# Kernel optimization log

Hardware: AMD Instinct MI355X
Metric: run time of the kernel (lower is better)

## Reference

```python
import jax, jax.numpy as jnp
import numpy as np

B, C, T, V, H = 128, 128, 64, 25, 4
EPS = 1e-5


def _bn(x, g, b, m, v):
    # eval-mode BatchNorm2d over channel axis 1 of [B,C,T,V]
    inv = g / jnp.sqrt(v + EPS)
    return x * inv[:, None, None] + (b - m * inv)[:, None, None]


def setup_inputs() -> dict:
    key = jax.random.key(0)
    ks = jax.random.split(key, 12)
    s = 0.05
    return {
        "x": jax.random.normal(ks[0], (B, C, T, V), jnp.float32),
        "bn0_gamma": jnp.ones((C,), jnp.float32),
        "bn0_beta": jnp.zeros((C,), jnp.float32),
        "bn0_mean": jax.random.normal(ks[1], (C,), jnp.float32) * s,
        "bn0_var": jnp.abs(jax.random.normal(ks[2], (C,), jnp.float32)) + 1.0,
        "conv1_w": jax.random.normal(ks[3], (2 * C, C), jnp.float32) * (1.0 / np.sqrt(C)),
        "conv1_b": jax.random.normal(ks[4], (2 * C,), jnp.float32) * s,
        "bn1_gamma": jnp.ones((C,), jnp.float32),
        "bn1_beta": jnp.zeros((C,), jnp.float32),
        "bn1_mean": jax.random.normal(ks[5], (C,), jnp.float32) * s,
        "bn1_var": jnp.abs(jax.random.normal(ks[6], (C,), jnp.float32)) + 1.0,
        "bn2_gamma": jnp.ones((C,), jnp.float32),
        "bn2_beta": jnp.zeros((C,), jnp.float32),
        "bn2_mean": jax.random.normal(ks[7], (C,), jnp.float32) * s,
        "bn2_var": jnp.abs(jax.random.normal(ks[8], (C,), jnp.float32)) + 1.0,
        "shared_topology": jnp.tile(jnp.eye(V, dtype=jnp.float32)[None], (H, 1, 1))
                           + jax.random.normal(ks[9], (H, V, V), jnp.float32) * s,
        "spatial_weight": jax.random.normal(ks[10], (H, V, V), jnp.float32) * s,
        "conv2_w": jax.random.normal(ks[11], (C, C), jnp.float32) * (1.0 / np.sqrt(C)),
        "conv2_b": jnp.zeros((C,), jnp.float32),
    }


def reference(x, bn0_gamma, bn0_beta, bn0_mean, bn0_var,
              conv1_w, conv1_b,
              bn1_gamma, bn1_beta, bn1_mean, bn1_var,
              bn2_gamma, bn2_beta, bn2_mean, bn2_var,
              shared_topology, spatial_weight,
              conv2_w, conv2_b):
    residual = x
    h = _bn(x, bn0_gamma, bn0_beta, bn0_mean, bn0_var)
    # conv1: 1x1 conv C -> 2C
    h = jnp.einsum('oc,bctv->botv', conv1_w, h) + conv1_b[None, :, None, None]
    h = jax.nn.gelu(h, approximate=False)  # torch nn.GELU default is exact
    z1, z2 = jnp.split(h, 2, axis=1)
    z1 = _bn(z1, bn1_gamma, bn1_beta, bn1_mean, bn1_var)
    z2 = _bn(z2, bn2_gamma, bn2_beta, bn2_mean, bn2_var)
    D = C // H
    z1 = z1.reshape(B, H, D, T, V)
    z2 = z2.reshape(B, H, D, T, V)
    y1 = jnp.einsum('huv,bhdtv->bhdtu', shared_topology, z1)
    attn = jnp.einsum('huv,bhdtv->bhdtu', spatial_weight, z2)
    y = (y1 + z1 * attn).reshape(B, C, T, V)
    y = jnp.einsum('oc,bctv->botv', conv2_w, y) + conv2_b[None, :, None, None]
    return jax.nn.relu(y + residual)
```

## Files before the change

### kernel.cpp

```cpp
#include <hip/hip_runtime.h>
#include <math.h>

#define C_   128
#define T_   64
#define V_   25
#define TV   1600
#define CTV  204800
#define EPS  1e-5f
#define TT   2
#define HS   136
#define ZS   72
#define RSZ  9216

typedef __bf16 bf16x8 __attribute__((ext_vector_type(8)));
typedef __bf16 bf16x4 __attribute__((ext_vector_type(4)));
typedef float  f32x4  __attribute__((ext_vector_type(4)));

__device__ __forceinline__ float gelu_exact(float x) {
  float y = fabsf(x) * 0.70710678118654752440f;
  float t = __builtin_amdgcn_rcpf(fmaf(0.47047f, y, 1.0f));
  float p = fmaf(0.7478556f, t, -0.0958798f);
  p = fmaf(p, t, 0.3480242f);
  p = p * t;
  float s = p * __expf(-y * y);
  float hxs = 0.5f * x * s;
  return x >= 0.0f ? x - hxs : hxs;
}

__global__ __launch_bounds__(256) void prep_pack(
    const float* __restrict__ W1, const float* __restrict__ W2,
    const float* __restrict__ topo, const float* __restrict__ spat,
    const float* __restrict__ b1,
    const float* __restrict__ bn0g, const float* __restrict__ bn0b,
    const float* __restrict__ bn0m, const float* __restrict__ bn0v,
    const float* __restrict__ bn1g, const float* __restrict__ bn1b,
    const float* __restrict__ bn1m, const float* __restrict__ bn1v,
    const float* __restrict__ bn2g, const float* __restrict__ bn2b,
    const float* __restrict__ bn2m, const float* __restrict__ bn2v,
    __bf16* __restrict__ W1p, __bf16* __restrict__ W2p, __bf16* __restrict__ Sp,
    float* __restrict__ b1a, float* __restrict__ binv, float* __restrict__ badd) {
  if (blockIdx.x == 128) {
    int o = threadIdx.x;
    float acc = b1[o];
    for (int c = 0; c < 128; ++c) {
      float inv = bn0g[c] * rsqrtf(bn0v[c] + EPS);
      float add = fmaf(-bn0m[c], inv, bn0b[c]);
      acc = fmaf(W1[o * 128 + c], add, acc);
    }
    b1a[o] = acc;
    float g, bb, m, vv;
    if (o < 128) { g = bn1g[o]; bb = bn1b[o]; m = bn1m[o]; vv = bn1v[o]; }
    else { int c = o - 128; g = bn2g[c]; bb = bn2b[c]; m = bn2m[c]; vv = bn2v[c]; }
    float inv = g * rsqrtf(vv + EPS);
    binv[o] = inv;
    badd[o] = fmaf(-m, inv, bb);
    return;
  }
  int i = blockIdx.x * 256 + threadIdx.x;
  if (i < 32768) {
    int j = i & 7, l = (i >> 3) & 63, ks = (i >> 9) & 3, ot = i >> 11;
    int o = ot * 16 + (l & 15);
    int c = ks * 32 + ((l >> 4) << 3) + j;
    float inv = bn0g[c] * rsqrtf(bn0v[c] + EPS);
    W1p[i] = (__bf16)(W1[o * 128 + c] * inv);
  }
  if (i < 16384) {
    int j = i & 7, l = (i >> 3) & 63, ks = (i >> 9) & 3, ot = i >> 11;
    int o = ot * 16 + (l & 15);
    int c = ks * 32 + ((l >> 4) << 3) + j;
    W2p[i] = (__bf16)W2[o * 128 + c];
  }
  if (i < 8192) {
    int j = i & 7, l = (i >> 3) & 63, ut = (i >> 9) & 1, mat = (i >> 10) & 1, h = i >> 11;
    int u = ut * 16 + (l & 15);
    int v = ((l >> 4) << 3) + j;
    const float* src = mat ? spat : topo;
    Sp[i] = (__bf16)((u < 25 && v < 25) ? src[h * 625 + u * 25 + v] : 0.0f);
  }
}


__device__ __forceinline__ void p0_stage(__bf16* hT, const float* xb, int tid) {
  const int c = tid >> 2, q = tid & 3;
  const int t = q & 1, vh = q >> 1;
  const float* xr = xb + c * TV + t * V_;
  const int v0 = vh * 12;
  float xv[13];
  #pragma unroll
  for (int i = 0; i < 13; ++i) xv[i] = xr[v0 + i];
  #pragma unroll
  for (int i = 0; i < 13; ++i)
    hT[(t * 32 + v0 + i) * HS + c] = (__bf16)xv[i];
}

__device__ __forceinline__ void conv1_mfma(const __bf16* hT, const __bf16* W1p,
    int wave, int lane, int lr, int lg, float bv0, float bv1, f32x4 acc[2][4]) {
  #pragma unroll
  for (int mt = 0; mt < 4; ++mt) {
    acc[0][mt] = f32x4{bv0, bv0, bv0, bv0};
    acc[1][mt] = f32x4{bv1, bv1, bv1, bv1};
  }
  #pragma unroll
  for (int ks = 0; ks < 4; ++ks) {
    bf16x8 ah[4];
    #pragma unroll
    for (int mt = 0; mt < 4; ++mt)
      ah[mt] = *reinterpret_cast<const bf16x8*>(&hT[(mt * 16 + lr) * HS + ks * 32 + lg * 8]);
    #pragma unroll
    for (int nt = 0; nt < 2; ++nt) {
      bf16x8 bw = *reinterpret_cast<const bf16x8*>(W1p + (((wave * 2 + nt) * 4 + ks) << 9) + lane * 8);
      #pragma unroll
      for (int mt = 0; mt < 4; ++mt)
        acc[nt][mt] = __builtin_amdgcn_mfma_f32_16x16x32_bf16(ah[mt], bw, acc[nt][mt], 0, 0, 0);
    }
  }
}

__device__ __forceinline__ void gelu_epi(const f32x4 acc[2][4], __bf16* z1, __bf16* z2,
    int wave, int lg, int o0, float inv0, float add0, float inv1, float add1) {
  __bf16* zdst = (wave < 4) ? z1 : z2;
  #pragma unroll
  for (int nt = 0; nt < 2; ++nt) {
    const float inv = nt ? inv1 : inv0;
    const float add = nt ? add1 : add0;
    const int orow = (o0 + nt * 16) & 127;
    #pragma unroll
    for (int mt = 0; mt < 4; ++mt) {
      bf16x4 pk;
      #pragma unroll
      for (int r = 0; r < 4; ++r) {
        int v = ((mt & 1) * 16) + lg * 4 + r;
        float z = fmaf(gelu_exact(acc[nt][mt][r]), inv, add);
        pk[r] = (v < V_) ? (__bf16)z : (__bf16)0.0f;
      }
      *reinterpret_cast<bf16x4*>(zdst + orow * ZS + mt * 16 + lg * 4) = pk;
    }
  }
}

__device__ __forceinline__ void spatial_mfma(const __bf16* z1, const __bf16* z2,
    const bf16x8 at0, const bf16x8 at1, const bf16x8 as0, const bf16x8 as1,
    int cbase, int lr, int lg, float yv[2][2][4]) {
  f32x4 accY[2][2] = {}, accA[2][2] = {};
  #pragma unroll
  for (int t = 0; t < 2; ++t) {
    bf16x8 az1 = *reinterpret_cast<const bf16x8*>(&z1[(cbase + lr) * ZS + t * 32 + lg * 8]);
    bf16x8 az2 = *reinterpret_cast<const bf16x8*>(&z2[(cbase + lr) * ZS + t * 32 + lg * 8]);
    accY[0][t] = __builtin_amdgcn_mfma_f32_16x16x32_bf16(az1, at0, accY[0][t], 0, 0, 0);
    accY[1][t] = __builtin_amdgcn_mfma_f32_16x16x32_bf16(az1, at1, accY[1][t], 0, 0, 0);
    accA[0][t] = __builtin_amdgcn_mfma_f32_16x16x32_bf16(az2, as0, accA[0][t], 0, 0, 0);
    accA[1][t] = __builtin_amdgcn_mfma_f32_16x16x32_bf16(az2, as1, accA[1][t], 0, 0, 0);
  }
  #pragma unroll
  for (int ut = 0; ut < 2; ++ut) {
    const int u = ut * 16 + lr;
    #pragma unroll
    for (int t = 0; t < 2; ++t)
      #pragma unroll
      for (int r = 0; r < 4; ++r) {
        const int c = cbase + lg * 4 + r;
        float z1u = (float)z1[c * ZS + t * 32 + u];
        yv[ut][t][r] = fmaf(z1u, accA[ut][t][r], accY[ut][t][r]);
      }
  }
}

__device__ __forceinline__ void p2_store(const float yv[2][2][4], __bf16* yT,
    int cbase, int lr, int lg) {
  #pragma unroll
  for (int ut = 0; ut < 2; ++ut)
    #pragma unroll
    for (int t = 0; t < 2; ++t) {
      const int row = t * 32 + ut * 16 + lr;
      bf16x4 pk;
      #pragma unroll
      for (int r = 0; r < 4; ++r) pk[r] = (__bf16)yv[ut][t][r];
      *reinterpret_cast<bf16x4*>(yT + row * HS + cbase + lg * 4) = pk;
    }
}

__device__ __forceinline__ void conv2_mfma(const __bf16* yT, const __bf16* W2p,
    int wave, int lane, int lr, int lg, const f32x4 bv2q, f32x4 acc2[4]) {
  #pragma unroll
  for (int n4 = 0; n4 < 4; ++n4) acc2[n4] = bv2q;
  #pragma unroll
  for (int ks = 0; ks < 4; ++ks) {
    bf16x8 af = *reinterpret_cast<const bf16x8*>(W2p + ((wave * 4 + ks) << 9) + lane * 8);
    #pragma unroll
    for (int n4 = 0; n4 < 4; ++n4) {
      bf16x8 ay = *reinterpret_cast<const bf16x8*>(&yT[(n4 * 16 + lr) * HS + ks * 32 + lg * 8]);
      acc2[n4] = __builtin_amdgcn_mfma_f32_16x16x32_bf16(af, ay, acc2[n4], 0, 0, 0);
    }
  }
}

__device__ __forceinline__ void p3_store(const f32x4 acc2[4], const float* xb,
    float* ob, int wave, int lr, int lg) {
  #pragma unroll
  for (int n4 = 0; n4 < 4; ++n4) {
    const int col = n4 * 16 + lr;
    const int t = col >> 5, u = col & 31;
    if (u < V_) {
      #pragma unroll
      for (int r = 0; r < 4; ++r) {
        const int o = wave * 16 + lg * 4 + r;
        const int off = o * TV + t * V_ + u;
        ob[off] = fmaxf(acc2[n4][r] + xb[off], 0.0f);
      }
    }
  }
}

__global__ __launch_bounds__(512, 4) void fused_v16(
    const float* __restrict__ x, const float* __restrict__ b2,
    const __bf16* __restrict__ W1p, const __bf16* __restrict__ W2p,
    const __bf16* __restrict__ Sp,
    const float* __restrict__ b1a, const float* __restrict__ binv,
    const float* __restrict__ badd,
    float* __restrict__ out) {
  __shared__ __bf16 sR[4 * RSZ];
  __bf16* RA = sR;
  __bf16* RB = sR + RSZ;
  __bf16* RC = sR + 2 * RSZ;
  __bf16* RD = sR + 3 * RSZ;

  const int hw = blockIdx.x;
  const int pb = (hw & 7) * 256 + (hw >> 3);
  const int b  = pb >> 4;
  const int tb0 = (pb & 15) * 2;
  const float* xb0 = x   + (size_t)b * CTV + tb0 * (TT * V_);
  float*       ob0 = out + (size_t)b * CTV + tb0 * (TT * V_);
  const float* xb1 = xb0 + TT * V_;
  float*       ob1 = ob0 + TT * V_;
  const int tid  = threadIdx.x;
  const int wave = tid >> 6, lane = tid & 63;
  const int lr = lane & 15, lg = lane >> 4;

  const int o0 = wave * 32 + lr;
  const float bv1a0 = b1a[o0], bv1a1 = b1a[o0 + 16];
  const float inv0 = binv[o0], add0 = badd[o0];
  const float inv1 = binv[o0 + 16], add1 = badd[o0 + 16];
  const f32x4 bv2q = *reinterpret_cast<const f32x4*>(b2 + wave * 16 + lg * 4);
  const int h2 = wave >> 1, ch = wave & 1;
  const int cbase = h2 * 32 + ch * 16;
  const bf16x8 at0 = *reinterpret_cast<const bf16x8*>(Sp + (((h2 * 2 + 0) * 2 + 0) << 9) + lane * 8);
  const bf16x8 at1 = *reinterpret_cast<const bf16x8*>(Sp + (((h2 * 2 + 0) * 2 + 1) << 9) + lane * 8);
  const bf16x8 as0 = *reinterpret_cast<const bf16x8*>(Sp + (((h2 * 2 + 1) * 2 + 0) << 9) + lane * 8);
  const bf16x8 as1 = *reinterpret_cast<const bf16x8*>(Sp + (((h2 * 2 + 1) * 2 + 1) << 9) + lane * 8);

  f32x4 acc[2][4];
  f32x4 acc2[4];
  float yv[2][2][4];

  p0_stage(RA, xb0, tid);
  __syncthreads();

  conv1_mfma(RA, W1p, wave, lane, lr, lg, bv1a0, bv1a1, acc);
  gelu_epi(acc, RC, RD, wave, lg, o0, inv0, add0, inv1, add1);
  __syncthreads();

  spatial_mfma(RC, RD, at0, at1, as0, as1, cbase, lr, lg, yv);
  p0_stage(RA, xb1, tid);
  p2_store(yv, RB, cbase, lr, lg);
  __syncthreads();

  conv2_mfma(RB, W2p, wave, lane, lr, lg, bv2q, acc2);
  conv1_mfma(RA, W1p, wave, lane, lr, lg, bv1a0, bv1a1, acc);
  gelu_epi(acc, RC, RD, wave, lg, o0, inv0, add0, inv1, add1);
  p3_store(acc2, xb0, ob0, wave, lr, lg);
  __syncthreads();

  spatial_mfma(RC, RD, at0, at1, as0, as1, cbase, lr, lg, yv);
  p2_store(yv, RB, cbase, lr, lg);
  __syncthreads();

  conv2_mfma(RB, W2p, wave, lane, lr, lg, bv2q, acc2);
  p3_store(acc2, xb1, ob1, wave, lr, lg);
}

extern "C" void kernel_launch(void* const* d_in, const int* in_sizes, int n_in,
                              void* d_out, int out_size, void* d_ws, size_t ws_size,
                              hipStream_t stream) {
  const float* x    = (const float*)d_in[0];
  const float* bn0g = (const float*)d_in[1];
  const float* bn0b = (const float*)d_in[2];
  const float* bn0m = (const float*)d_in[3];
  const float* bn0v = (const float*)d_in[4];
  const float* W1   = (const float*)d_in[5];
  const float* b1   = (const float*)d_in[6];
  const float* bn1g = (const float*)d_in[7];
  const float* bn1b = (const float*)d_in[8];
  const float* bn1m = (const float*)d_in[9];
  const float* bn1v = (const float*)d_in[10];
  const float* bn2g = (const float*)d_in[11];
  const float* bn2b = (const float*)d_in[12];
  const float* bn2m = (const float*)d_in[13];
  const float* bn2v = (const float*)d_in[14];
  const float* topo = (const float*)d_in[15];
  const float* spat = (const float*)d_in[16];
  const float* W2   = (const float*)d_in[17];
  const float* b2   = (const float*)d_in[18];
  float* out = (float*)d_out;

  __bf16* W1p = (__bf16*)d_ws;
  __bf16* W2p = W1p + 32768;
  __bf16* Sp  = W2p + 16384;
  float*  b1a  = (float*)((char*)d_ws + 114688);
  float*  binv = b1a + 256;
  float*  badd = binv + 256;

  prep_pack<<<129, 256, 0, stream>>>(W1, W2, topo, spat, b1,
                                     bn0g, bn0b, bn0m, bn0v,
                                     bn1g, bn1b, bn1m, bn1v,
                                     bn2g, bn2b, bn2m, bn2v,
                                     W1p, W2p, Sp, b1a, binv, badd);
  fused_v16<<<2048, 512, 0, stream>>>(
      x, b2, W1p, W2p, Sp, b1a, binv, badd, out);
}
```

Measured before the change: 99.41 us.

## Make blocks persistent over four tile pairs with a pipelined loop

Each block now loops over four consecutive pairs of time tiles instead of one pair, with grid reduced from 2048 to 512 blocks. The next tile's input staging is overlapped with the previous tile's conv2/store phase across loop iterations. This amortizes per-block setup (bias, BN and spatial-weight register loads, pipeline fill) but cuts resident blocks per CU and thus latency hiding. Address swizzling of blocks is dropped in favor of contiguous quarter-batch chunks.

Result: slower. 275.2 us (+176.8%).

```diff
diff --git a/kernel.cpp b/kernel.cpp
--- a/kernel.cpp
+++ b/kernel.cpp
@@ -211,7 +211,7 @@
   }
 }
 
-__global__ __launch_bounds__(512, 4) void fused_v16(
+__global__ __launch_bounds__(512, 4) void fused_v17(
     const float* __restrict__ x, const float* __restrict__ b2,
     const __bf16* __restrict__ W1p, const __bf16* __restrict__ W2p,
     const __bf16* __restrict__ Sp,
@@ -224,14 +224,11 @@
   __bf16* RC = sR + 2 * RSZ;
   __bf16* RD = sR + 3 * RSZ;
 
-  const int hw = blockIdx.x;
-  const int pb = (hw & 7) * 256 + (hw >> 3);
-  const int b  = pb >> 4;
-  const int tb0 = (pb & 15) * 2;
-  const float* xb0 = x   + (size_t)b * CTV + tb0 * (TT * V_);
-  float*       ob0 = out + (size_t)b * CTV + tb0 * (TT * V_);
-  const float* xb1 = xb0 + TT * V_;
-  float*       ob1 = ob0 + TT * V_;
+  const int qb   = blockIdx.x;
+  const int b    = qb >> 2;
+  const int quad = qb & 3;
+  const float* xq = x   + (size_t)b * CTV + quad * (16 * V_);
+  float*       oq = out + (size_t)b * CTV + quad * (16 * V_);
   const int tid  = threadIdx.x;
   const int wave = tid >> 6, lane = tid & 63;
   const int lr = lane & 15, lg = lane >> 4;
@@ -248,34 +245,56 @@
   const bf16x8 as0 = *reinterpret_cast<const bf16x8*>(Sp + (((h2 * 2 + 1) * 2 + 0) << 9) + lane * 8);
   const bf16x8 as1 = *reinterpret_cast<const bf16x8*>(Sp + (((h2 * 2 + 1) * 2 + 1) << 9) + lane * 8);
 
-  f32x4 acc[2][4];
-  f32x4 acc2[4];
-  float yv[2][2][4];
-
-  p0_stage(RA, xb0, tid);
+  p0_stage(RA, xq, tid);
   __syncthreads();
 
-  conv1_mfma(RA, W1p, wave, lane, lr, lg, bv1a0, bv1a1, acc);
-  gelu_epi(acc, RC, RD, wave, lg, o0, inv0, add0, inv1, add1);
-  __syncthreads();
-
-  spatial_mfma(RC, RD, at0, at1, as0, as1, cbase, lr, lg, yv);
-  p0_stage(RA, xb1, tid);
-  p2_store(yv, RB, cbase, lr, lg);
-  __syncthreads();
-
-  conv2_mfma(RB, W2p, wave, lane, lr, lg, bv2q, acc2);
-  conv1_mfma(RA, W1p, wave, lane, lr, lg, bv1a0, bv1a1, acc);
-  gelu_epi(acc, RC, RD, wave, lg, o0, inv0, add0, inv1, add1);
-  p3_store(acc2, xb0, ob0, wave, lr, lg);
-  __syncthreads();
-
-  spatial_mfma(RC, RD, at0, at1, as0, as1, cbase, lr, lg, yv);
-  p2_store(yv, RB, cbase, lr, lg);
-  __syncthreads();
-
-  conv2_mfma(RB, W2p, wave, lane, lr, lg, bv2q, acc2);
-  p3_store(acc2, xb1, ob1, wave, lr, lg);
+  #pragma unroll 1
+  for (int i = 0; i < 4; ++i) {
+    const float* xt0 = xq + i * (2 * TT * V_);
+    float*       ot0 = oq + i * (2 * TT * V_);
+    const float* xt1 = xt0 + TT * V_;
+    float*       ot1 = ot0 + TT * V_;
+
+    {
+      f32x4 acc[2][4];
+      conv1_mfma(RA, W1p, wave, lane, lr, lg, bv1a0, bv1a1, acc);
+      gelu_epi(acc, RC, RD, wave, lg, o0, inv0, add0, inv1, add1);
+    }
+    __syncthreads();
+
+    {
+      float yv[2][2][4];
+      spatial_mfma(RC, RD, at0, at1, as0, as1, cbase, lr, lg, yv);
+      p0_stage(RA, xt1, tid);
+      p2_store(yv, RB, cbase, lr, lg);
+    }
+    __syncthreads();
+
+    {
+      f32x4 acc2[4];
+      f32x4 acc[2][4];
+      conv2_mfma(RB, W2p, wave, lane, lr, lg, bv2q, acc2);
+      conv1_mfma(RA, W1p, wave, lane, lr, lg, bv1a0, bv1a1, acc);
+      gelu_epi(acc, RC, RD, wave, lg, o0, inv0, add0, inv1, add1);
+      p3_store(acc2, xt0, ot0, wave, lr, lg);
+    }
+    __syncthreads();
+
+    {
+      float yv[2][2][4];
+      spatial_mfma(RC, RD, at0, at1, as0, as1, cbase, lr, lg, yv);
+      p2_store(yv, RB, cbase, lr, lg);
+    }
+    __syncthreads();
+
+    {
+      f32x4 acc2[4];
+      conv2_mfma(RB, W2p, wave, lane, lr, lg, bv2q, acc2);
+      if (i < 3) p0_stage(RA, xt1 + TT * V_, tid);
+      p3_store(acc2, xt1, ot1, wave, lr, lg);
+    }
+    if (i < 3) __syncthreads();
+  }
 }
 
 extern "C" void kernel_launch(void* const* d_in, const int* in_sizes, int n_in,
@@ -314,6 +333,6 @@
                                      bn1g, bn1b, bn1m, bn1v,
                                      bn2g, bn2b, bn2m, bn2v,
                                      W1p, W2p, Sp, b1a, binv, badd);
-  fused_v16<<<2048, 512, 0, stream>>>(
+  fused_v17<<<512, 512, 0, stream>>>(
       x, b2, W1p, W2p, Sp, b1a, binv, badd, out);
 }
```
